# Performance work log

Measured on AMD Instinct MI355X. Metric: run time of the kernel, lower is better.

The kernel has to match this reference:

```python
import jax, jax.numpy as jnp
import numpy as np
from jax import lax

N, D = 16384, 512
E_SPEC, E_SHARED = 8, 2


def setup_inputs() -> dict:
    key = jax.random.key(0)
    ks = jax.random.split(key, 7)
    return {
        "x": jax.random.normal(ks[0], (N, D), dtype=jnp.float32),
        "spec_router_logits": jax.random.normal(ks[1], (N, E_SPEC), dtype=jnp.float32),
        "shared_router_logits": jax.random.normal(ks[2], (N, E_SHARED), dtype=jnp.float32),
        "spec_W": jax.random.normal(ks[3], (E_SPEC, D, D), dtype=jnp.float32) * 0.02,
        "spec_b": jax.random.normal(ks[4], (E_SPEC, D), dtype=jnp.float32) * 0.02,
        "shared_W": jax.random.normal(ks[5], (E_SHARED, D, D), dtype=jnp.float32) * 0.02,
        "shared_b": jax.random.normal(ks[6], (E_SHARED, D), dtype=jnp.float32) * 0.02,
        "top_k": 2,
    }


def reference(x, spec_router_logits, shared_router_logits, spec_W, spec_b, shared_W, shared_b, top_k):
    n, e_spec = spec_router_logits.shape
    # --- specific experts: top-k routing with renormalized weights ---
    spec_probs = jax.nn.softmax(spec_router_logits, axis=1)          # [N, E_spec]
    topk_w, topk_idx = lax.top_k(spec_probs, top_k)                  # [N, K]
    topk_w = topk_w / (jnp.sum(topk_w, axis=1, keepdims=True) + 1e-6)
    # dense per-token per-expert weight matrix (zero for unselected), matching
    # the original dense mask-accumulate loop
    weights = jnp.zeros((n, e_spec), dtype=spec_probs.dtype)
    weights = weights.at[jnp.arange(n)[:, None], topk_idx].add(topk_w)  # [N, E_spec]
    # dense eval of all specific experts (Linear d->d), then weighted combine
    spec_outs = jnp.einsum('nd,edf->enf', x, spec_W) + spec_b[:, None, :]  # [E,N,D]
    spec_out = jnp.einsum('ne,enf->nf', weights, spec_outs)                # [N,D]
    # --- shared experts: soft combine over softmax probs ---
    shared_probs = jax.nn.softmax(shared_router_logits, axis=1)           # [N, E_shared]
    shared_outs = jnp.einsum('nd,edf->enf', x, shared_W) + shared_b[:, None, :]
    shared_out = jnp.einsum('ne,enf->nf', shared_probs, shared_outs)
    return spec_out + shared_out
```

## Files before the change

kernel.cpp:

```cpp
#include <hip/hip_runtime.h>
#include <stdint.h>

typedef unsigned short ushort_t;
typedef __attribute__((ext_vector_type(8))) short short8;
typedef __attribute__((ext_vector_type(4))) float f32x4;
typedef __attribute__((ext_vector_type(4))) unsigned int u32x4;

#define TOK  16384
#define DIM  512
#define NPAIR 64
#define MAXTILES 156

__device__ __forceinline__ unsigned short f2bf(float f) {
  union { float f; uint32_t u; } v; v.f = f;
  uint32_t u = v.u;
  uint32_t r = (u + 0x7fffu + ((u >> 16) & 1u)) >> 16;
  return (unsigned short)r;
}

__global__ void k_prep(const float* __restrict__ wspec, const float* __restrict__ wsh,
                       ushort_t* __restrict__ wt,
                       const float* __restrict__ sl, const float* __restrict__ shl,
                       float* __restrict__ w4, int* __restrict__ pairid,
                       int* __restrict__ cnt) {
  if (blockIdx.z < 10) {
    __shared__ float t[32][33];
    int e = blockIdx.z;
    const float* src = (e < 8) ? (wspec + e * DIM * DIM) : (wsh + (e - 8) * DIM * DIM);
    int tx = threadIdx.x, ty = threadIdx.y;
    int d = blockIdx.y * 32 + ty, f = blockIdx.x * 32 + tx;
    t[ty][tx] = src[d * DIM + f];
    __syncthreads();
    int fo = blockIdx.x * 32 + ty, dd = blockIdx.y * 32 + tx;
    wt[(size_t)e * DIM * DIM + fo * DIM + dd] = f2bf(t[tx][ty]);
    return;
  }
  int blk = blockIdx.y * 16 + blockIdx.x;
  if (blk >= 16) return;
  __shared__ int h[NPAIR];
  int tid = threadIdx.y * 32 + threadIdx.x;
  int n = blk * 1024 + tid;
  if (tid < NPAIR) h[tid] = 0;
  __syncthreads();
  float l[8];
  float m = -1e30f;
#pragma unroll
  for (int i = 0; i < 8; ++i) { l[i] = sl[n*8 + i]; m = fmaxf(m, l[i]); }
  float s = 0.f;
#pragma unroll
  for (int i = 0; i < 8; ++i) { l[i] = expf(l[i] - m); s += l[i]; }
  float inv = 1.f / s;
#pragma unroll
  for (int i = 0; i < 8; ++i) l[i] *= inv;
  int i1 = 0; float v1 = l[0];
#pragma unroll
  for (int i = 1; i < 8; ++i) if (l[i] > v1) { v1 = l[i]; i1 = i; }
  int i2 = -1; float v2 = -1.f;
#pragma unroll
  for (int i = 0; i < 8; ++i) if (i != i1 && l[i] > v2) { v2 = l[i]; i2 = i; }
  float rs = 1.f / (v1 + v2 + 1e-6f);
  float w1 = v1 * rs, w2 = v2 * rs;
  int pmin, pmax; float wa, wb;
  if (i1 < i2) { pmin = i1; pmax = i2; wa = w1; wb = w2; }
  else         { pmin = i2; pmax = i1; wa = w2; wb = w1; }
  float s0 = shl[n*2], s1 = shl[n*2 + 1];
  float mm = fmaxf(s0, s1);
  float e0 = expf(s0 - mm), e1 = expf(s1 - mm);
  float si = 1.f / (e0 + e1);
  w4[n*4 + 0] = wa;
  w4[n*4 + 1] = wb;
  w4[n*4 + 2] = e0 * si;
  w4[n*4 + 3] = e1 * si;
  int p = pmin * 8 + pmax;
  pairid[n] = p;
  atomicAdd(&h[p], 1);
  __syncthreads();
  if (tid < NPAIR && h[tid]) atomicAdd(&cnt[tid], h[tid]);
}

__global__ void k_scan(const int* __restrict__ cnt, int* __restrict__ off,
                       int* __restrict__ cursor, int* __restrict__ tsinfo,
                       int* __restrict__ tileinfo, ushort_t* __restrict__ idx) {
  int l = threadIdx.x;
  int c = cnt[l];
  int t = (c + 127) >> 7;
  int sc = c, st = t;
#pragma unroll
  for (int d = 1; d < 64; d <<= 1) {
    int vc = __shfl_up(sc, d, 64);
    int vt = __shfl_up(st, d, 64);
    if (l >= d) { sc += vc; st += vt; }
  }
  int offv = sc - c, tsv = st - t;
  off[l] = offv; cursor[l] = offv;
  if (l == 63) tsinfo[64] = st;
  for (int q = 0; q < t; ++q) tileinfo[tsv + q] = (l << 16) | q;
  for (int i = l; i < 128; i += 64) idx[TOK + i] = 0;
}

__global__ void k_fill(const int* __restrict__ pairid, int* __restrict__ cursor,
                       ushort_t* __restrict__ idx) {
  __shared__ int hcnt[NPAIR];
  __shared__ int hbase[NPAIR];
  int tid = threadIdx.x;
  int n = blockIdx.x * 256 + tid;
  if (tid < NPAIR) hcnt[tid] = 0;
  __syncthreads();
  int p = pairid[n];
  int r = atomicAdd(&hcnt[p], 1);
  __syncthreads();
  if (tid < NPAIR && hcnt[tid]) hbase[tid] = atomicAdd(&cursor[tid], hcnt[tid]);
  __syncthreads();
  idx[hbase[p] + r] = (ushort_t)n;
}

__global__ void k_gather(const float* __restrict__ x, const ushort_t* __restrict__ idx,
                         ushort_t* __restrict__ xg) {
  int row = blockIdx.x * 4 + (threadIdx.x >> 6);
  int lane = threadIdx.x & 63;
  int t = (int)idx[row];
  const float* src = x + (size_t)t * DIM + lane * 8;
  f32x4 v0 = *(const f32x4*)src;
  f32x4 v1 = *(const f32x4*)(src + 4);
  u32x4 o;
  o[0] = (uint32_t)f2bf(v0[0]) | ((uint32_t)f2bf(v0[1]) << 16);
  o[1] = (uint32_t)f2bf(v0[2]) | ((uint32_t)f2bf(v0[3]) << 16);
  o[2] = (uint32_t)f2bf(v1[0]) | ((uint32_t)f2bf(v1[1]) << 16);
  o[3] = (uint32_t)f2bf(v1[2]) | ((uint32_t)f2bf(v1[3]) << 16);
  *(u32x4*)(xg + (size_t)row * DIM + lane * 8) = o;
}

__global__ __launch_bounds__(256, 3)
void k_moe(const ushort_t* __restrict__ xg, const ushort_t* __restrict__ wt,
           const float* __restrict__ w4, const ushort_t* __restrict__ idx,
           const int* __restrict__ off, const int* __restrict__ cnt,
           const int* __restrict__ tsinfo, const int* __restrict__ tileinfo,
           const float* __restrict__ bspec, const float* __restrict__ bsh,
           float* __restrict__ out) {
  __shared__ ushort_t aB[2][8192];
  __shared__ ushort_t bB[2][4096];
  __shared__ float wLT[4 * 128];
  __shared__ float wRT[4 * 128];

  const int tid  = threadIdx.x;
  const int lane = tid & 63;
  const int w    = tid >> 6;
  const int wr   = w >> 1, wc = w & 1;

  int bx  = blockIdx.x;
  int r   = bx >> 3, cdx = bx & 7;
  if (r >= tsinfo[64]) return;
  int info = tileinfo[r];
  int p = info >> 16, tstart = info & 0xffff;
  const int base = off[p] + (tstart << 7);
  int cl = cnt[p] - (tstart << 7); if (cl > 128) cl = 128;
  const int e0 = p >> 3, e1 = p & 7;
  const int tcol = cdx << 6;

  int soffA[4];
#pragma unroll
  for (int q = 0; q < 4; ++q) {
    int pp  = (q << 12) + tid * 16;
    int row = pp >> 7;
    int kb  = (pp & 127) ^ ((row & 7) << 4);
    soffA[q] = row * DIM + (kb >> 1);
  }
  const ushort_t* aSrc = xg + (size_t)base * DIM;
  const ushort_t* bSrc = wt + (size_t)tcol * DIM;

  auto stageA = [&](int ks) {
#pragma unroll
    for (int q = 0; q < 4; ++q)
      __builtin_amdgcn_global_load_lds(
          (const __attribute__((address_space(1))) void*)(aSrc + (ks << 6) + soffA[q]),
          (__attribute__((address_space(3))) void*)((char*)&aB[ks & 1][0] + (q << 12) + tid * 16),
          16, 0, 0);
  };
  auto stageB = [&](int ks, int jn) {
    int e = (jn == 0) ? e0 : (jn == 1) ? e1 : (jn == 2) ? 8 : 9;
    const ushort_t* b = bSrc + ((size_t)e << 18) + (ks << 6);
#pragma unroll
    for (int q = 0; q < 2; ++q)
      __builtin_amdgcn_global_load_lds(
          (const __attribute__((address_space(1))) void*)(b + soffA[q]),
          (__attribute__((address_space(3))) void*)((char*)&bB[jn & 1][0] + (q << 12) + tid * 16),
          16, 0, 0);
  };

  stageA(0);
  stageB(0, 0);

  for (int i = tid; i < 512; i += 256) {
    int j = i >> 7, rs = i & 127;
    float wa = 1.f, wb = 1.f;
    if (rs < cl) {
      int t = (int)idx[base + rs];
      wa = w4[t * 4 + j];
      wb = w4[t * 4 + ((j + 1) & 3)];
    }
    wLT[i] = wa;
    wRT[i] = wa / wb;
  }

  int aRd[4][2], bRd[2][2];
#pragma unroll
  for (int i = 0; i < 4; ++i) {
    int row = wr * 64 + i * 16 + (lane & 15);
#pragma unroll
    for (int ksl = 0; ksl < 2; ++ksl) {
      int kb = ((ksl << 6) + ((lane >> 4) << 4)) ^ ((row & 7) << 4);
      aRd[i][ksl] = row * 128 + kb;
    }
  }
#pragma unroll
  for (int i = 0; i < 2; ++i) {
    int col = wc * 32 + i * 16 + (lane & 15);
#pragma unroll
    for (int ksl = 0; ksl < 2; ++ksl) {
      int kb = ((ksl << 6) + ((lane >> 4) << 4)) ^ ((col & 7) << 4);
      bRd[i][ksl] = col * 128 + kb;
    }
  }

  f32x4 acc[4][2];
#pragma unroll
  for (int a = 0; a < 4; ++a)
#pragma unroll
    for (int b = 0; b < 2; ++b) acc[a][b] = (f32x4){0.f, 0.f, 0.f, 0.f};

  __syncthreads();

  auto computeStep = [&](const ushort_t* abp, const ushort_t* bbp) {
    const char* ab = (const char*)abp;
    const char* bb = (const char*)bbp;
#pragma unroll
    for (int ksl = 0; ksl < 2; ++ksl) {
      u32x4 af[4], bf[2];
#pragma unroll
      for (int i = 0; i < 4; ++i) af[i] = *(const u32x4*)(ab + aRd[i][ksl]);
#pragma unroll
      for (int i = 0; i < 2; ++i) bf[i] = *(const u32x4*)(bb + bRd[i][ksl]);
#pragma unroll
      for (int rb = 0; rb < 4; ++rb) {
        short8 a8 = __builtin_bit_cast(short8, af[rb]);
#pragma unroll
        for (int cb = 0; cb < 2; ++cb) {
          short8 b8 = __builtin_bit_cast(short8, bf[cb]);
          acc[rb][cb] = __builtin_amdgcn_mfma_f32_16x16x32_bf16(a8, b8, acc[rb][cb], 0, 0, 0);
        }
      }
    }
  };
  auto telescope = [&](int j) {
#pragma unroll
    for (int rb = 0; rb < 4; ++rb) {
      int rl = wr * 64 + rb * 16 + ((lane >> 4) << 2);
      f32x4 rv = *(const f32x4*)&wRT[(j << 7) + rl];
      acc[rb][0] *= rv;
      acc[rb][1] *= rv;
    }
  };

#define WAITV0 asm volatile("s_waitcnt vmcnt(0)" ::: "memory")
#define WAITV4 asm volatile("s_waitcnt vmcnt(4)" ::: "memory")
#define RBAR   do { __builtin_amdgcn_s_barrier(); __builtin_amdgcn_sched_barrier(0); } while (0)

#pragma unroll 1
  for (int ks = 0; ks < 8; ++ks) {
    const ushort_t* ab = &aB[ks & 1][0];
    WAITV0; RBAR;
    stageB(ks, 1);
    computeStep(ab, &bB[0][0]);
    telescope(0);
    WAITV0; RBAR;
    stageB(ks, 2);
    computeStep(ab, &bB[1][0]);
    telescope(1);
    WAITV0; RBAR;
    stageB(ks, 3);
    if (ks < 7) stageA(ks + 1);
    computeStep(ab, &bB[0][0]);
    telescope(2);
    if (ks < 7) { WAITV4; } else { WAITV0; }
    RBAR;
    if (ks < 7) stageB(ks + 1, 0);
    computeStep(ab, &bB[1][0]);
    if (ks < 7) telescope(3);
  }

#pragma unroll
  for (int rb = 0; rb < 4; ++rb) {
    int rl = wr * 64 + rb * 16 + ((lane >> 4) << 2);
    f32x4 wv[4];
#pragma unroll
    for (int j = 0; j < 4; ++j) wv[j] = *(const f32x4*)&wLT[(j << 7) + rl];
    int tok[4]; bool pr[4];
#pragma unroll
    for (int q = 0; q < 4; ++q) {
      int rs = rl + q; pr[q] = rs < cl;
      tok[q] = pr[q] ? (int)idx[base + rs] : 0;
    }
#pragma unroll
    for (int cb = 0; cb < 2; ++cb) {
      int cloc = wc * 32 + cb * 16 + (lane & 15);
      f32x4 v = acc[rb][cb] * wv[3];
#pragma unroll
      for (int j = 0; j < 4; ++j) {
        int e = (j == 0) ? e0 : (j == 1) ? e1 : (j == 2) ? 8 : 9;
        float bj = (e < 8) ? bspec[e * DIM + tcol + cloc] : bsh[(e - 8) * DIM + tcol + cloc];
        v += wv[j] * bj;
      }
#pragma unroll
      for (int q = 0; q < 4; ++q)
        if (pr[q]) out[(size_t)tok[q] * DIM + tcol + cloc] = v[q];
    }
  }
#undef WAITV0
#undef WAITV4
#undef RBAR
}

extern "C" void kernel_launch(void* const* d_in, const int* in_sizes, int n_in,
                              void* d_out, int out_size, void* d_ws, size_t ws_size,
                              hipStream_t stream) {
  (void)in_sizes; (void)n_in; (void)out_size; (void)ws_size;
  const float* x   = (const float*)d_in[0];
  const float* srl = (const float*)d_in[1];
  const float* shl = (const float*)d_in[2];
  const float* sW  = (const float*)d_in[3];
  const float* sb  = (const float*)d_in[4];
  const float* hW  = (const float*)d_in[5];
  const float* hb  = (const float*)d_in[6];
  float* out = (float*)d_out;

  char* ws = (char*)d_ws;
  float*    w4     = (float*)ws;     ws += TOK * 4 * 4;
  int*      pairid = (int*)ws;       ws += TOK * 4;
  ushort_t* idx    = (ushort_t*)ws;  ws += (TOK + 128) * 2 + 256;
  int*      cntp   = (int*)ws;       ws += NPAIR * 4;
  int*      offp   = (int*)ws;       ws += NPAIR * 4;
  int*      curp   = (int*)ws;       ws += NPAIR * 4;
  int*      tsp    = (int*)ws;       ws += (NPAIR + 1) * 4;
  int*      tinfo  = (int*)ws;       ws += MAXTILES * 4 + 208;
  ushort_t* xg     = (ushort_t*)ws;  ws += (size_t)(TOK + 128) * DIM * 2;
  ushort_t* wt     = (ushort_t*)ws;

  hipMemsetAsync(cntp, 0, NPAIR * sizeof(int), stream);
  dim3 tb(32, 32, 1), tg(16, 16, 11);
  k_prep<<<tg, tb, 0, stream>>>(sW, hW, wt, srl, shl, w4, pairid, cntp);
  k_scan<<<1, 64, 0, stream>>>(cntp, offp, curp, tsp, tinfo, idx);
  k_fill<<<TOK / 256, 256, 0, stream>>>(pairid, curp, idx);
  k_gather<<<(TOK + 128) / 4, 256, 0, stream>>>(x, idx, xg);
  k_moe<<<MAXTILES * 8, 256, 0, stream>>>(xg, wt, w4, idx, offp, cntp, tsp, tinfo,
                                          sb, hb, out);
}
```

Measured before the change: 97.63 us.

## Deepen expert-weight prefetch to four LDS buffers with partial vmcnt waits

The B-operand LDS buffer grows from two slots to four, one per expert (two routed, two shared). Each weight tile is now staged several compute steps ahead, and the waits use partial vmcnt counts instead of draining all outstanding loads, so more global-to-LDS traffic overlaps the MFMA work. In exchange, LDS per block grows and launch bounds drop from 3 to 2 blocks per CU, which lowers occupancy. The vmcnt counts have to match the issue order exactly, which makes the schedule fragile.

```diff
diff --git a/kernel.cpp b/kernel.cpp
--- a/kernel.cpp
+++ b/kernel.cpp
@@ -130,7 +130,7 @@
   *(u32x4*)(xg + (size_t)row * DIM + lane * 8) = o;
 }
 
-__global__ __launch_bounds__(256, 3)
+__global__ __launch_bounds__(256, 2)
 void k_moe(const ushort_t* __restrict__ xg, const ushort_t* __restrict__ wt,
            const float* __restrict__ w4, const ushort_t* __restrict__ idx,
            const int* __restrict__ off, const int* __restrict__ cnt,
@@ -138,7 +138,7 @@
            const float* __restrict__ bspec, const float* __restrict__ bsh,
            float* __restrict__ out) {
   __shared__ ushort_t aB[2][8192];
-  __shared__ ushort_t bB[2][4096];
+  __shared__ ushort_t bB[4][4096];
   __shared__ float wLT[4 * 128];
   __shared__ float wRT[4 * 128];
 
@@ -176,19 +176,20 @@
           (__attribute__((address_space(3))) void*)((char*)&aB[ks & 1][0] + (q << 12) + tid * 16),
           16, 0, 0);
   };
-  auto stageB = [&](int ks, int jn) {
-    int e = (jn == 0) ? e0 : (jn == 1) ? e1 : (jn == 2) ? 8 : 9;
+  auto stageB = [&](int e, int ks, int buf) {
     const ushort_t* b = bSrc + ((size_t)e << 18) + (ks << 6);
 #pragma unroll
     for (int q = 0; q < 2; ++q)
       __builtin_amdgcn_global_load_lds(
           (const __attribute__((address_space(1))) void*)(b + soffA[q]),
-          (__attribute__((address_space(3))) void*)((char*)&bB[jn & 1][0] + (q << 12) + tid * 16),
+          (__attribute__((address_space(3))) void*)((char*)&bB[buf][0] + (q << 12) + tid * 16),
           16, 0, 0);
   };
 
   stageA(0);
-  stageB(0, 0);
+  stageB(e0, 0, 0);
+  stageB(e1, 0, 1);
+  stageB(8,  0, 2);
 
   for (int i = tid; i < 512; i += 256) {
     int j = i >> 7, rs = i & 127;
@@ -230,9 +231,7 @@
 
   __syncthreads();
 
-  auto computeStep = [&](const ushort_t* abp, const ushort_t* bbp) {
-    const char* ab = (const char*)abp;
-    const char* bb = (const char*)bbp;
+  auto computeStep = [&](const char* ab, const char* bb) {
 #pragma unroll
     for (int ksl = 0; ksl < 2; ++ksl) {
       u32x4 af[4], bf[2];
@@ -261,32 +260,33 @@
     }
   };
 
-#define WAITV0 asm volatile("s_waitcnt vmcnt(0)" ::: "memory")
-#define WAITV4 asm volatile("s_waitcnt vmcnt(4)" ::: "memory")
-#define RBAR   do { __builtin_amdgcn_s_barrier(); __builtin_amdgcn_sched_barrier(0); } while (0)
+#define WAITN(n) asm volatile("s_waitcnt vmcnt(" #n ")" ::: "memory")
+#define RBAR     do { __builtin_amdgcn_s_barrier(); __builtin_amdgcn_sched_barrier(0); } while (0)
 
 #pragma unroll 1
   for (int ks = 0; ks < 8; ++ks) {
-    const ushort_t* ab = &aB[ks & 1][0];
-    WAITV0; RBAR;
-    stageB(ks, 1);
-    computeStep(ab, &bB[0][0]);
+    const char* ab = (const char*)&aB[ks & 1][0];
+    WAITN(4); RBAR;
+    stageB(9, ks, 3);
+    computeStep(ab, (const char*)&bB[0][0]);
     telescope(0);
-    WAITV0; RBAR;
-    stageB(ks, 2);
-    computeStep(ab, &bB[1][0]);
+    WAITN(4); RBAR;
+    if (ks < 7) { stageB(e0, ks + 1, 0); stageA(ks + 1); }
+    computeStep(ab, (const char*)&bB[1][0]);
     telescope(1);
-    WAITV0; RBAR;
-    stageB(ks, 3);
-    if (ks < 7) stageA(ks + 1);
-    computeStep(ab, &bB[0][0]);
+    if (ks < 7) { WAITN(8); } else { WAITN(2); }
+    RBAR;
+    if (ks < 7) stageB(e1, ks + 1, 1);
+    computeStep(ab, (const char*)&bB[2][0]);
     telescope(2);
-    if (ks < 7) { WAITV4; } else { WAITV0; }
+    if (ks < 7) { WAITN(8); } else { WAITN(0); }
     RBAR;
-    if (ks < 7) stageB(ks + 1, 0);
-    computeStep(ab, &bB[1][0]);
+    if (ks < 7) stageB(8, ks + 1, 2);
+    computeStep(ab, (const char*)&bB[3][0]);
     if (ks < 7) telescope(3);
   }
+#undef WAITN
+#undef RBAR
 
 #pragma unroll
   for (int rb = 0; rb < 4; ++rb) {
@@ -315,9 +315,6 @@
         if (pr[q]) out[(size_t)tok[q] * DIM + tcol + cloc] = v[q];
     }
   }
-#undef WAITV0
-#undef WAITV4
-#undef RBAR
 }
 
 extern "C" void kernel_launch(void* const* d_in, const int* in_sizes, int n_in,
```

Result: slower. 108.4 us (+11.0%).
